# Kernel tuning notes

Hardware: AMD Instinct MI355X
Metric: run time of the kernel (lower is better)

The kernel has to match this reference:

```python
import jax, jax.numpy as jnp
import numpy as np

EPS = 1e-5  # BatchNorm eps (torch default)

def _wq(w):
    # W8A16 fake-quant: per-output-channel symmetric int8 quantize + dequantize
    s = jnp.max(jnp.abs(w), axis=tuple(range(1, w.ndim)), keepdims=True) / 127.0
    s = jnp.maximum(s, 1e-8)
    q = jnp.clip(jnp.round(w / s), -128.0, 127.0)
    return q * s

def _conv(x, w, b, pad):
    y = jax.lax.conv_general_dilated(x, _wq(w), (1, 1), [(pad, pad), (pad, pad)],
                                     dimension_numbers=('NCHW', 'OIHW', 'NCHW'))
    return y + b[None, :, None, None]

def _bn(x, g, b, m, v):
    sh = (1, -1, 1, 1) if x.ndim == 4 else (1, -1)
    inv = jax.lax.rsqrt(v + EPS)
    return (x - m.reshape(sh)) * (inv * g).reshape(sh) + b.reshape(sh)

def _pool(x):
    return jax.lax.reduce_window(x, -jnp.inf, jax.lax.max, (1, 1, 2, 2), (1, 1, 2, 2), 'VALID')

def _ht(x):
    return jnp.clip(x, -1.0, 1.0)

def _linear(x, w, b):
    return x @ _wq(w).T + b

def setup_inputs() -> dict:
    key = jax.random.key(0)
    ks = iter(jax.random.split(key, 64))
    def rn(shape, s=0.05):
        return jax.random.normal(next(ks), shape, jnp.float32) * s
    d = {}
    d['x'] = jax.random.normal(next(ks), (1024, 1, 28, 28), jnp.float32)
    convs = [(1, 32, 5), (32, 64, 5), (64, 128, 3), (128, 256, 3), (256, 256, 1)]
    for i, (ci, co, k) in enumerate(convs, 1):
        d[f'w{i}'] = rn((co, ci, k, k), 0.1)
        d[f'b{i}'] = rn((co,))
        d[f'g{i}'] = jnp.ones((co,), jnp.float32)
        d[f'be{i}'] = jnp.zeros((co,), jnp.float32)
        d[f'mu{i}'] = rn((co,))
        d[f'va{i}'] = jax.random.uniform(next(ks), (co,), jnp.float32, 0.5, 1.5)
    fcs = [(2304, 1024), (1024, 512)]
    for i, (fi, fo) in enumerate(fcs, 1):
        d[f'fw{i}'] = rn((fo, fi), 0.05)
        d[f'fb{i}'] = rn((fo,))
        d[f'fg{i}'] = jnp.ones((fo,), jnp.float32)
        d[f'fbe{i}'] = jnp.zeros((fo,), jnp.float32)
        d[f'fmu{i}'] = rn((fo,))
        d[f'fva{i}'] = jax.random.uniform(next(ks), (fo,), jnp.float32, 0.5, 1.5)
    d['fw3'] = rn((10, 512), 0.05)
    d['fb3'] = rn((10,))
    return d

def reference(x, w1, b1, g1, be1, mu1, va1, w2, b2, g2, be2, mu2, va2,
              w3, b3, g3, be3, mu3, va3, w4, b4, g4, be4, mu4, va4,
              w5, b5, g5, be5, mu5, va5,
              fw1, fb1, fg1, fbe1, fmu1, fva1,
              fw2, fb2, fg2, fbe2, fmu2, fva2, fw3, fb3):
    h = _ht(_bn(_conv(x, w1, b1, 2), g1, be1, mu1, va1))                 # [B,32,28,28]
    h = _ht(_bn(_pool(_conv(h, w2, b2, 2)), g2, be2, mu2, va2))          # [B,64,14,14]
    h = _ht(_bn(_pool(_conv(h, w3, b3, 1)), g3, be3, mu3, va3))          # [B,128,7,7]
    h = _ht(_bn(_pool(_conv(h, w4, b4, 1)), g4, be4, mu4, va4))          # [B,256,3,3]
    h = _ht(_bn(_conv(h, w5, b5, 0), g5, be5, mu5, va5))                 # [B,256,3,3]
    h = h.reshape(h.shape[0], -1)                                        # [B,2304]
    h = _ht(_bn(_linear(h, fw1, fb1), fg1, fbe1, fmu1, fva1))            # [B,1024]
    h = _ht(_bn(_linear(h, fw2, fb2), fg2, fbe2, fmu2, fva2))            # [B,512]
    return _linear(h, fw3, fb3)                                          # [B,10]
```

## Files before the change

kernel.cpp:

```cpp
#include <hip/hip_runtime.h>
#include <hip/hip_bf16.h>
#include <math.h>


#define EPS 1e-5f

typedef __attribute__((ext_vector_type(8))) short bf16x8;
typedef __attribute__((ext_vector_type(4))) float f32x4;
typedef __attribute__((ext_vector_type(16))) float f32x16;
typedef __attribute__((ext_vector_type(4))) int i32x4;

__device__ __forceinline__ short f2bf(float f) {
  unsigned u = __builtin_bit_cast(unsigned, f);
  unsigned r = u + 0x7FFFu + ((u >> 16) & 1u);
  return (short)(r >> 16);
}
__device__ __forceinline__ float bf2f(short h) {
  unsigned u = ((unsigned)(unsigned short)h) << 16;
  return __builtin_bit_cast(float, u);
}
__device__ __forceinline__ int swz2(int pin) {
  return (pin ^ (pin >> 2) ^ (pin >> 5)) & 3;
}
__device__ __forceinline__ int swz3(int pin) {
  return (pin ^ (pin >> 2) ^ (pin >> 4)) & 7;
}
__device__ __forceinline__ float qclip(float w, float s) {
  return fminf(fmaxf(rintf(w / s), -128.f), 127.f);
}

struct PrepArgs {
  const float* w[8];
  short* dsth[8];
  float* dstf;
  float* sc;
  int sco[8];
  int cik[8];
  int kind[8];
  int KK[8];
  int CI[8];
  int OCCH[8];
  int KC[8];
  int cum[9];
};

__global__ __launch_bounds__(256) void prep_all(PrepArgs a) {
  int b = blockIdx.x;
  int t = 0;
  while (b >= a.cum[t + 1]) t++;
  int oc = b - a.cum[t];
  int cik = a.cik[t];
  const float* src = a.w[t] + (size_t)oc * cik;
  float m = 0.f;
  for (int i = threadIdx.x; i < cik; i += 256) m = fmaxf(m, fabsf(src[i]));
  #pragma unroll
  for (int o = 1; o < 64; o <<= 1) m = fmaxf(m, __shfl_xor(m, o));
  __shared__ float red[4];
  __shared__ float ssh;
  if ((threadIdx.x & 63) == 0) red[threadIdx.x >> 6] = m;
  __syncthreads();
  if (threadIdx.x == 0) {
    m = fmaxf(fmaxf(red[0], red[1]), fmaxf(red[2], red[3]));
    float s = fmaxf(m / 127.0f, 1e-8f);
    ssh = s;
    a.sc[a.sco[t] + oc] = s;
  }
  __syncthreads();
  const float s = ssh;
  const int kind = a.kind[t];
  short* dst = a.dsth[t];
  if (kind == 0) {
    for (int tt = threadIdx.x; tt < 32; tt += 256) {
      float q = (tt < 25) ? qclip(src[tt], s) : 0.f;
      dst[(((oc >> 4) * 4 + (tt >> 3)) * 16 + (oc & 15)) * 8 + (tt & 7)] = f2bf(q);
    }
  } else if (kind == 1) {
    const int KK = a.KK[t], CI = a.CI[t], OCCH = a.OCCH[t];
    const int NT32 = OCCH >> 5, KS16 = CI >> 4;
    const int chunk = oc / OCCH, ocl = oc - chunk * OCCH;
    const int nt = ocl >> 5, n32 = ocl & 31;
    for (int idx = threadIdx.x; idx < cik; idx += 256) {
      int ci = idx / KK, kk = idx - ci * KK;
      float q = qclip(src[idx], s);
      int ks = ci >> 4, hh = (ci >> 3) & 1, j = ci & 7;
      size_t d = ((((size_t)(chunk * KK + kk) * NT32 + nt) * KS16 + ks) * 64 +
                  hh * 32 + n32) * 8 + j;
      dst[d] = f2bf(q);
    }
  } else if (kind == 2) {
    const int KK = a.KK[t], CI = a.CI[t], OCCH = a.OCCH[t];
    const int NTC = OCCH >> 4, KS = CI >> 5;
    const int chunk = oc / OCCH, ocl = oc - chunk * OCCH;
    const int ntl = ocl >> 4, mr = ocl & 15;
    for (int idx = threadIdx.x; idx < cik; idx += 256) {
      int ci = idx / KK, kk = idx - ci * KK;
      float q = qclip(src[idx], s);
      int ks = ci >> 5, qq = (ci >> 3) & 3, j = ci & 7;
      size_t d = ((((((size_t)(chunk * KK + kk) * NTC + ntl) * KS + ks) * 4 + qq) *
                   16 + mr)) * 8 + j;
      dst[d] = f2bf(q);
    }
  } else if (kind == 3) {
    const int KC = a.KC[t];
    const int nblk = oc >> 6, ntl = (oc >> 4) & 3, mr = oc & 15;
    for (int k = threadIdx.x; k < cik; k += 256) {
      float q = qclip(src[k], s);
      size_t d = ((((((size_t)nblk * KC + (k >> 7)) * 4 + ntl) * 4 + ((k >> 5) & 3)) *
                   4 + ((k >> 3) & 3)) * 16 + mr) * 8 + (k & 7);
      dst[d] = f2bf(q);
    }
  } else {
    for (int k = threadIdx.x; k < cik; k += 256)
      a.dstf[(size_t)oc * cik + k] = qclip(src[k], s) * s;
  }
}

struct BnArgs {
  const float* p[7][5];
  const float* wsc;
  float* ab;
  int C[7];
  int abo[7];
  int sco[7];
  int cum[8];
};

__global__ __launch_bounds__(256) void bn_all(BnArgs a) {
  int i = blockIdx.x * 256 + threadIdx.x;
  if (i >= a.cum[7]) return;
  int t = 0;
  while (i >= a.cum[t + 1]) t++;
  int c = i - a.cum[t];
  float A = a.p[t][1][c] / sqrtf(a.p[t][4][c] + EPS);
  float B = (a.p[t][0][c] - a.p[t][3][c]) * A + a.p[t][2][c];
  a.ab[a.abo[t] + c] = A * a.wsc[a.sco[t] + c];
  a.ab[a.abo[t] + a.C[t] + c] = B;
}

__global__ __launch_bounds__(448, 2) void conv1_mfma(
    const float* __restrict__ x, const short* __restrict__ wb1,
    const float* __restrict__ ab, short* __restrict__ out) {
  __shared__ __align__(16) float spad[1024];
  __shared__ __align__(16) short sim[784 * 32];
  __shared__ __align__(16) short sw1[1024];
  const int tid = threadIdx.x;
  const int img = blockIdx.x;
  for (int i = tid; i < 1024; i += 448) spad[i] = 0.f;
  for (int i = tid; i < 1024; i += 448) sw1[i] = wb1[i];
  __syncthreads();
  for (int i = tid; i < 784; i += 448)
    spad[(i / 28 + 2) * 32 + (i % 28) + 2] = x[(size_t)img * 784 + i];
  __syncthreads();
  for (int p = tid; p < 784; p += 448) {
    const int py = p / 28, px = p - py * 28;
    const float* sp = &spad[py * 32 + px];
    short v[32];
    #pragma unroll
    for (int ty = 0; ty < 5; ++ty)
      #pragma unroll
      for (int tx = 0; tx < 5; ++tx)
        v[ty * 5 + tx] = f2bf(sp[ty * 32 + tx]);
    #pragma unroll
    for (int j = 25; j < 32; ++j) v[j] = 0;
    #pragma unroll
    for (int j = 0; j < 4; ++j)
      *(bf16x8*)&sim[p * 32 + j * 8] = *(const bf16x8*)&v[j * 8];
  }
  __syncthreads();
  const int lane = tid & 63, wv = tid >> 6;
  const int mrow = lane & 15, quad = lane >> 4;
  f32x4 acc[7][2];
  #pragma unroll
  for (int i = 0; i < 7; ++i) {
    acc[i][0] = (f32x4){0.f, 0.f, 0.f, 0.f};
    acc[i][1] = (f32x4){0.f, 0.f, 0.f, 0.f};
  }
  #pragma unroll
  for (int i = 0; i < 7; ++i) {
    const int mt = wv * 7 + i;
    const bf16x8 a = *(const bf16x8*)&sim[(mt * 16 + mrow) * 32 + quad * 8];
    #pragma unroll
    for (int nt = 0; nt < 2; ++nt) {
      const bf16x8 b = *(const bf16x8*)&sw1[(nt * 4 + quad) * 128 + mrow * 8];
      acc[i][nt] = __builtin_amdgcn_mfma_f32_16x16x32_bf16(a, b, acc[i][nt], 0, 0, 0);
    }
  }
  #pragma unroll
  for (int i = 0; i < 7; ++i) {
    const int mt = wv * 7 + i;
    #pragma unroll
    for (int nt = 0; nt < 2; ++nt) {
      const int oc = nt * 16 + mrow;
      const float A = ab[oc], Bc = ab[32 + oc];
      #pragma unroll
      for (int r = 0; r < 4; ++r) {
        const int p = mt * 16 + quad * 4 + r;
        float v = fminf(fmaxf(acc[i][nt][r] * A + Bc, -1.f), 1.f);
        out[((size_t)img * 784 + p) * 32 + oc] = f2bf(v);
      }
    }
  }
}

__global__ __launch_bounds__(256, 2) void conv2_half(
    const short* __restrict__ in, const short* __restrict__ wfrag,
    const float* __restrict__ ab, short* __restrict__ out) {
  constexpr int S = 4;
  constexpr int RS = 32;
  __shared__ __align__(16) short simg[18 * 32 * 32];
  __shared__ __align__(16) short sw[2][10240];
  const int tid = threadIdx.x;
  const int img = blockIdx.x >> 1, half = blockIdx.x & 1;
  const int lane = tid & 63, wv = tid >> 6;
  const int l31 = lane & 31, h = lane >> 5;

  {
    const int padrow0 = half ? 16 : 0;
    const int vrow0 = half ? 0 : 2;
    for (int c = tid; c < 512; c += 256) {
      int hp = c >> 2, blk = c & 3;
      int pin;
      if (hp < 64) {
        pin = (padrow0 + (hp >> 5)) * RS + (hp & 31);
      } else {
        int r = (hp - 64) >> 2, cc = (hp - 64) & 3;
        int col = (cc < 2) ? cc : (28 + cc);
        pin = (vrow0 + r) * RS + col;
      }
      ((i32x4*)simg)[pin * S + blk] = (i32x4){0, 0, 0, 0};
    }
  }
  {
    const i32x4* gin = (const i32x4*)(in + ((size_t)img * 784 + half * 12 * 28) * 32);
    const int vrow0 = half ? 0 : 2;
    for (int c = tid; c < 1792; c += 256) {
      int ps = c >> 2, blk = c & 3;
      int pin = (vrow0 + ps / 28) * RS + ps % 28 + 2;
      ((i32x4*)simg)[pin * S + (blk ^ swz2(pin))] = gin[c];
    }
  }

  int pinb[4], ppb[4];
  bool uv2[4];
  #pragma unroll
  for (int i = 0; i < 4; ++i) {
    int u = wv + i * 4;
    uv2[i] = u < 13;
    int m = u * 32 + l31;
    int ppl = m >> 2, cd = m & 3;
    bool ok = uv2[i] && (ppl < 98);
    int pr = ppl / 14, pc = ppl - pr * 14;
    int ygl = (half * 7 + pr) * 2 + (cd >> 1);
    int yll = ygl - (half * 14 - 2);
    int xc = pc * 2 + (cd & 1) + 2;
    pinb[i] = ok ? (yll * RS + xc) : (2 * RS + 2);
    ppb[i] = u * 8;
  }

  f32x16 acc[4][2];
  #pragma unroll
  for (int i = 0; i < 4; ++i)
    #pragma unroll
    for (int nt = 0; nt < 2; ++nt)
      #pragma unroll
      for (int e = 0; e < 16; ++e) acc[i][nt][e] = 0.f;

  i32x4 wreg[5];
  {
    const i32x4* ws0 = (const i32x4*)wfrag;
    #pragma unroll
    for (int u2 = 0; u2 < 5; ++u2) wreg[u2] = ws0[tid + u2 * 256];
    #pragma unroll
    for (int u2 = 0; u2 < 5; ++u2) ((i32x4*)sw[0])[tid + u2 * 256] = wreg[u2];
  }

  for (int tg = 0; tg < 5; ++tg) {
    __syncthreads();
    if (tg < 4) {
      const i32x4* ws = (const i32x4*)(wfrag + (size_t)(tg + 1) * 10240);
      #pragma unroll
      for (int u2 = 0; u2 < 5; ++u2) wreg[u2] = ws[tid + u2 * 256];
    }
    const short* swb = sw[tg & 1];
    const int dy = tg - 2;
    #pragma unroll
    for (int tt = 0; tt < 5; ++tt) {
      const int tp = dy * RS + (tt - 2);
      int pin[4], sx4[4];
      #pragma unroll
      for (int i = 0; i < 4; ++i) {
        pin[i] = pinb[i] + tp;
        sx4[i] = swz2(pin[i]);
      }
      #pragma unroll
      for (int ks = 0; ks < 2; ++ks) {
        bf16x8 af[4];
        #pragma unroll
        for (int i = 0; i < 4; ++i)
          af[i] = *(const bf16x8*)&simg[pin[i] * 32 + (((ks * 2 + h) ^ sx4[i]) * 8)];
        #pragma unroll
        for (int nt = 0; nt < 2; ++nt) {
          const bf16x8 bf = *(const bf16x8*)&swb[(((tt * 2 + nt) * 2 + ks) * 64 + lane) * 8];
          #pragma unroll
          for (int i = 0; i < 4; ++i)
            acc[i][nt] = __builtin_amdgcn_mfma_f32_32x32x16_bf16(af[i], bf, acc[i][nt], 0, 0, 0);
        }
      }
    }
    if (tg < 4) {
      #pragma unroll
      for (int u2 = 0; u2 < 5; ++u2)
        ((i32x4*)sw[(tg + 1) & 1])[tid + u2 * 256] = wreg[u2];
    }
  }

  #pragma unroll
  for (int i = 0; i < 4; ++i) {
    #pragma unroll
    for (int nt = 0; nt < 2; ++nt) {
      const int oc = nt * 32 + l31;
      const float A = ab[oc], Bc = ab[64 + oc];
      #pragma unroll
      for (int g = 0; g < 4; ++g) {
        const int ppo = ppb[i] + 2 * g + h;
        if (uv2[i] && ppo < 98) {
          float mx = fmaxf(fmaxf(acc[i][nt][g * 4 + 0], acc[i][nt][g * 4 + 1]),
                           fmaxf(acc[i][nt][g * 4 + 2], acc[i][nt][g * 4 + 3]));
          float v = fminf(fmaxf(mx * A + Bc, -1.f), 1.f);
          out[((size_t)img * 196 + half * 98 + ppo) * 64 + oc] = f2bf(v);
        }
      }
    }
  }
}

__global__ __launch_bounds__(256, 2) void conv3_pad(
    const short* __restrict__ in, const short* __restrict__ wfrag,
    const float* __restrict__ ab, short* __restrict__ out) {
  constexpr int S = 8, RS = 16;
  __shared__ __align__(16) short simg[2 * 256 * 64];
  __shared__ __align__(16) short sw[2][4096];
  const int tid = threadIdx.x;
  const int img0 = blockIdx.x * 2;
  const int lane = tid & 63, wv = tid >> 6;
  const int l31 = lane & 31, h = lane >> 5;

  for (int c = tid; c < 960; c += 256) {
    int blk = c & 7, hp0 = c >> 3;
    int il = hp0 >= 60 ? 1 : 0, hp = hp0 - il * 60;
    int pin;
    if (hp < 32) pin = (hp >> 4) * 15 * RS + (hp & 15);
    else {
      int r = ((hp - 32) >> 1) + 1, cc = ((hp - 32) & 1) * 15;
      pin = r * RS + cc;
    }
    ((i32x4*)simg)[(il * 256 + pin) * S + blk] = (i32x4){0, 0, 0, 0};
  }
  {
    const i32x4* gin = (const i32x4*)(in + (size_t)img0 * 196 * 64);
    for (int c = tid; c < 3136; c += 256) {
      int il = c / 1568, r = c - il * 1568;
      int ps = r >> 3, blk = r & 7;
      int pin = (ps / 14 + 1) * RS + ps % 14 + 1;
      ((i32x4*)simg)[(il * 256 + pin) * S + (blk ^ swz3(pin))] = gin[c];
    }
  }

  int pinb[4], ppb[4], ilv[4];
  bool uv4[4];
  #pragma unroll
  for (int i = 0; i < 4; ++i) {
    int u = wv + i * 4;
    uv4[i] = u < 14;
    int uu = uv4[i] ? u : 0;
    int il = uu / 7, lt = uu - il * 7;
    int m = lt * 32 + l31, ppl = m >> 2, cd = m & 3;
    bool ok = uv4[i] && (ppl < 49);
    int py = ppl / 7, px = ppl - py * 7;
    int y = py * 2 + (cd >> 1), x = px * 2 + (cd & 1);
    pinb[i] = (ok ? ((y + 1) * RS + x + 1) : (RS + 1)) + il * 256;
    ilv[i] = il;
    ppb[i] = lt * 8;
  }

  f32x16 acc[4][2];
  #pragma unroll
  for (int i = 0; i < 4; ++i)
    #pragma unroll
    for (int nt = 0; nt < 2; ++nt)
      #pragma unroll
      for (int e = 0; e < 16; ++e) acc[i][nt][e] = 0.f;

  i32x4 wreg[2];
  {
    const i32x4* ws0 = (const i32x4*)wfrag;
    wreg[0] = ws0[tid];
    wreg[1] = ws0[tid + 256];
    ((i32x4*)sw[0])[tid] = wreg[0];
    ((i32x4*)sw[0])[tid + 256] = wreg[1];
  }

  for (int s = 0; s < 18; ++s) {
    __syncthreads();
    if (s < 17) {
      const i32x4* ws = (const i32x4*)(wfrag + (size_t)(s + 1) * 4096);
      wreg[0] = ws[tid];
      wreg[1] = ws[tid + 256];
    }
    const short* swb = sw[s & 1];
    const int t = s % 9;
    const int tp = (t / 3 - 1) * RS + (t % 3 - 1);
    int pin[4], sx4[4];
    #pragma unroll
    for (int i = 0; i < 4; ++i) {
      pin[i] = pinb[i] + tp;
      sx4[i] = swz3(pin[i]);
    }
    #pragma unroll
    for (int ks = 0; ks < 4; ++ks) {
      bf16x8 af[4];
      #pragma unroll
      for (int i = 0; i < 4; ++i)
        af[i] = *(const bf16x8*)&simg[pin[i] * 64 + (((ks * 2 + h) ^ sx4[i]) * 8)];
      #pragma unroll
      for (int nt = 0; nt < 2; ++nt) {
        const bf16x8 bf = *(const bf16x8*)&swb[((nt * 4 + ks) * 64 + lane) * 8];
        #pragma unroll
        for (int i = 0; i < 4; ++i)
          acc[i][nt] = __builtin_amdgcn_mfma_f32_32x32x16_bf16(af[i], bf, acc[i][nt], 0, 0, 0);
      }
    }
    if (s < 17) {
      ((i32x4*)sw[(s + 1) & 1])[tid] = wreg[0];
      ((i32x4*)sw[(s + 1) & 1])[tid + 256] = wreg[1];
    }
    if (t == 8) {
      const int ch = s / 9;
      #pragma unroll
      for (int i = 0; i < 4; ++i) {
        #pragma unroll
        for (int nt = 0; nt < 2; ++nt) {
          const int oc = ch * 64 + nt * 32 + l31;
          const float A = ab[oc], Bc = ab[128 + oc];
          #pragma unroll
          for (int g = 0; g < 4; ++g) {
            const int ppo = ppb[i] + 2 * g + h;
            if (uv4[i] && ppo < 49) {
              float mx = fmaxf(fmaxf(acc[i][nt][g * 4 + 0], acc[i][nt][g * 4 + 1]),
                               fmaxf(acc[i][nt][g * 4 + 2], acc[i][nt][g * 4 + 3]));
              float v = fminf(fmaxf(mx * A + Bc, -1.f), 1.f);
              out[((size_t)(img0 + ilv[i]) * 49 + ppo) * 128 + oc] = f2bf(v);
            }
          }
          #pragma unroll
          for (int e = 0; e < 16; ++e) acc[i][nt][e] = 0.f;
        }
      }
    }
  }
}

__global__ __launch_bounds__(512, 2) void conv4_mfma(
    const short* __restrict__ in,
    const short* __restrict__ wfrag,
    const float* __restrict__ ab,
    short* __restrict__ outH, short* __restrict__ outL) {
  constexpr int S = 16, NPIX = 49, PP = 9;
  __shared__ __align__(16) short simg[2 * NPIX * 128];
  __shared__ __align__(16) short swb[2][32768];
  const int tid = threadIdx.x;
  const int img0 = blockIdx.x * 2;
  const int lane = tid & 63, wv = tid >> 6;
  const int mrow = lane & 15, quad = lane >> 4;

  {
    const i32x4* gsrc = (const i32x4*)(in + (size_t)img0 * NPIX * 128);
    for (int c = tid; c < 2 * NPIX * S; c += 512) {
      int il = c / (NPIX * S);
      int r = c - il * (NPIX * S);
      int pix = r >> 4, blk = r & 15;
      ((i32x4*)simg)[il * NPIX * S + pix * S + (blk ^ (pix & 15))] = gsrc[c];
    }
    for (int u = tid; u < 4096; u += 512)
      ((i32x4*)swb[0])[u] = ((const i32x4*)wfrag)[u];
  }

  int yy[6], xx[6], ibs[6], ppo_[6], ilv[6];
  bool rv[6], pv[6];
  #pragma unroll
  for (int i = 0; i < 6; ++i) {
    int il = i / 3, lt = i - il * 3;
    int m = lt * 16 + mrow;
    int pp = m >> 2, cd = m & 3;
    rv[i] = pp < PP;
    int py = pp / 3, px = pp - py * 3;
    yy[i] = py * 2 + (cd >> 1);
    xx[i] = px * 2 + (cd & 1);
    ibs[i] = il * NPIX * S;
    ilv[i] = il;
    ppo_[i] = lt * 4 + quad;
    pv[i] = ppo_[i] < PP;
  }
  const int nt0 = wv, nt1 = wv + 8;
  f32x4 acc[6][2];
  #pragma unroll
  for (int i = 0; i < 6; ++i) {
    acc[i][0] = (f32x4){0.f, 0.f, 0.f, 0.f};
    acc[i][1] = (f32x4){0.f, 0.f, 0.f, 0.f};
  }
  __syncthreads();

  int dy = -1, dx = -1;
  for (int t = 0; t < 9; ++t) {
    const int buf = t & 1;
    if (t < 8) {
      const i32x4* wsrc = (const i32x4*)(wfrag + (size_t)(t + 1) * 32768);
      for (int u = tid; u < 4096; u += 512) ((i32x4*)swb[buf ^ 1])[u] = wsrc[u];
    }
    #pragma unroll
    for (int ks = 0; ks < 4; ++ks) {
      bf16x8 af[6];
      #pragma unroll
      for (int i = 0; i < 6; ++i) {
        int iy = yy[i] + dy, ix = xx[i] + dx;
        bool ok = rv[i] && (unsigned)iy < 7u && (unsigned)ix < 7u;
        int pin = iy * 7 + ix;
        int blk = (ks * 4 + quad) ^ (pin & 15);
        af[i] = ok ? *(const bf16x8*)&simg[(ibs[i] + pin * S + blk) * 8]
                   : (bf16x8){0, 0, 0, 0, 0, 0, 0, 0};
      }
      const bf16x8 b0 = *(const bf16x8*)&swb[buf][((nt0 * 4 + ks) * 4 + quad) * 128 + mrow * 8];
      const bf16x8 b1 = *(const bf16x8*)&swb[buf][((nt1 * 4 + ks) * 4 + quad) * 128 + mrow * 8];
      #pragma unroll
      for (int i = 0; i < 6; ++i) {
        acc[i][0] = __builtin_amdgcn_mfma_f32_16x16x32_bf16(af[i], b0, acc[i][0], 0, 0, 0);
        acc[i][1] = __builtin_amdgcn_mfma_f32_16x16x32_bf16(af[i], b1, acc[i][1], 0, 0, 0);
      }
    }
    dx++;
    if (dx == 2) { dx = -1; dy++; }
    __syncthreads();
  }

  #pragma unroll
  for (int i = 0; i < 6; ++i) {
    if (pv[i]) {
      #pragma unroll
      for (int nj = 0; nj < 2; ++nj) {
        const int oc = (nj ? nt1 : nt0) * 16 + mrow;
        const f32x4 a = acc[i][nj];
        float mx = fmaxf(fmaxf(a[0], a[1]), fmaxf(a[2], a[3]));
        float v = fminf(fmaxf(mx * ab[oc] + ab[256 + oc], -1.f), 1.f);
        const int m5 = (img0 + ilv[i]) * 9 + ppo_[i];
        size_t d = ((((((size_t)(m5 >> 6) * 2 + (oc >> 7)) * 4 + ((m5 >> 4) & 3)) * 4 +
                     ((oc >> 5) & 3)) * 4 + ((oc >> 3) & 3)) * 16 + (m5 & 15)) * 8 + (oc & 7);
        short hi = f2bf(v);
        outH[d] = hi;
        outL[d] = f2bf(v - bf2f(hi));
      }
    }
  }
}

template <int KC, int OUTMODE, int KC2, int NALL>
__global__ __launch_bounds__(256, 4) void fc_mfma(
    const short* __restrict__ Xh, const short* __restrict__ Xl,
    const short* __restrict__ Wf, const float* __restrict__ ab,
    float* __restrict__ outF, short* __restrict__ outH, short* __restrict__ outL) {
  const int tid = threadIdx.x;
  const int bn = blockIdx.x, bm = blockIdx.y;
  const int lane = tid & 63, wv = tid >> 6;
  const int mrow = lane & 15, quad = lane >> 4;
  f32x4 acc[4];
  #pragma unroll
  for (int nt = 0; nt < 4; ++nt) acc[nt] = (f32x4){0.f, 0.f, 0.f, 0.f};

  for (int kc = 0; kc < KC; ++kc) {
    const short* xb = Xh + (((size_t)bm * KC + kc) * 4 + wv) * 2048;
    const short* xlb = Xl + (((size_t)bm * KC + kc) * 4 + wv) * 2048;
    const short* wb = Wf + ((size_t)bn * KC + kc) * 8192;
    #pragma unroll
    for (int ks = 0; ks < 4; ++ks) {
      const int ao = ((ks * 4 + quad) * 16 + mrow) * 8;
      const bf16x8 ah = *(const bf16x8*)&xb[ao];
      const bf16x8 al = *(const bf16x8*)&xlb[ao];
      #pragma unroll
      for (int nt = 0; nt < 4; ++nt) {
        const bf16x8 b = *(const bf16x8*)&wb[(((nt * 4 + ks) * 4 + quad) * 16 + mrow) * 8];
        acc[nt] = __builtin_amdgcn_mfma_f32_16x16x32_bf16(ah, b, acc[nt], 0, 0, 0);
        acc[nt] = __builtin_amdgcn_mfma_f32_16x16x32_bf16(al, b, acc[nt], 0, 0, 0);
      }
    }
  }

  #pragma unroll
  for (int nt = 0; nt < 4; ++nt) {
    const int n = bn * 64 + nt * 16 + mrow;
    const float A = ab[n], Bc = ab[NALL + n];
    #pragma unroll
    for (int r = 0; r < 4; ++r) {
      const int m = bm * 64 + wv * 16 + quad * 4 + r;
      float v = fminf(fmaxf(acc[nt][r] * A + Bc, -1.f), 1.f);
      if (OUTMODE == 0) {
        size_t d = (((((((size_t)(m >> 6) * KC2 + (n >> 7)) * 4 + ((m >> 4) & 3)) * 4 +
                       ((n >> 5) & 3)) * 4 + ((n >> 3) & 3)) * 16 + (m & 15))) * 8 + (n & 7);
        short hi = f2bf(v);
        outH[d] = hi;
        outL[d] = f2bf(v - bf2f(hi));
      } else if (OUTMODE == 1) {
        outF[(size_t)m * NALL + n] = v;
      } else {
        const int imgq = m / 9, p = m - imgq * 9;
        const int k1 = n * 9 + p;
        size_t d = ((((((size_t)(imgq >> 6) * KC2 + (k1 >> 7)) * 4 + ((imgq >> 4) & 3)) * 4 +
                     ((k1 >> 5) & 3)) * 4 + ((k1 >> 3) & 3)) * 16 + (imgq & 15)) * 8 + (k1 & 7);
        short hi = f2bf(v);
        outH[d] = hi;
        outL[d] = f2bf(v - bf2f(hi));
      }
    }
  }
}

__global__ __launch_bounds__(256) void fc3_kernel(
    const float* __restrict__ X, const float* __restrict__ W,
    const float* __restrict__ bias, float* __restrict__ out) {
  __shared__ float ws[512 * 10 + 16];
  for (int li = threadIdx.x; li < 5120; li += 256) {
    int n = li / 512, k = li - n * 512;
    ws[k * 10 + n] = W[li];
  }
  __syncthreads();
  const int il = threadIdx.x >> 4, n = threadIdx.x & 15;
  const int img = blockIdx.x * 16 + il;
  if (n < 10) {
    const float4* xp = (const float4*)(X + (size_t)img * 512);
    float s = 0.f;
    for (int k4 = 0; k4 < 128; ++k4) {
      const float4 xv = xp[k4];
      const int k = k4 * 4;
      s += xv.x * ws[k * 10 + n];
      s += xv.y * ws[(k + 1) * 10 + n];
      s += xv.z * ws[(k + 2) * 10 + n];
      s += xv.w * ws[(k + 3) * 10 + n];
    }
    out[img * 10 + n] = s + bias[n];
  }
}

extern "C" void kernel_launch(void* const* d_in, const int* in_sizes, int n_in,
                              void* d_out, int out_size, void* d_ws, size_t ws_size,
                              hipStream_t stream) {
  (void)in_sizes; (void)n_in; (void)out_size; (void)ws_size;
  const float* x = (const float*)d_in[0];
  float* W = (float*)d_ws;

  float* wsc  = W + 0;
  float* ab   = W + 2304;
  float* fq3  = W + 6912;
  short* wb1  = (short*)(W + 12032);
  short* wb2  = (short*)(W + 12544);
  short* wb3  = (short*)(W + 38144);
  short* wb4  = (short*)(W + 75008);
  short* wb5  = (short*)(W + 222464);
  short* fqb1 = (short*)(W + 255232);
  short* fqb2 = (short*)(W + 1434880);
  short* h1   = (short*)(W + 1697024);
  short* h2   = (short*)(W + 14542080);
  short* h3   = (short*)(W + 20964608);
  short* h4h  = (short*)(W + 24175872);
  short* h4l  = (short*)(W + 25355520);
  short* h5h  = (short*)(W + 26535168);
  short* h5l  = (short*)(W + 27714816);
  short* f1h  = (short*)(W + 28894464);
  short* f1l  = (short*)(W + 29418752);
  float* f2   = W + 29943040;

  PrepArgs pa;
  const int widx[8] = {1, 7, 13, 19, 25, 31, 37, 43};
  short* pdst[8] = {wb1, wb2, wb3, wb4, wb5, fqb1, fqb2, nullptr};
  const int sco8[8] = {0, 32, 96, 224, 480, 736, 1760, 2272};
  const int cik8[8] = {25, 800, 576, 1152, 256, 2304, 1024, 512};
  const int co8[8] = {32, 64, 128, 256, 256, 1024, 512, 10};
  const int kind8[8] = {0, 1, 1, 2, 3, 3, 3, 4};
  const int KK8[8] = {25, 25, 9, 9, 1, 1, 1, 1};
  const int CI8[8] = {1, 32, 64, 128, 256, 2304, 1024, 512};
  const int OCCH8[8] = {32, 64, 64, 256, 256, 1024, 512, 10};
  const int KC8[8] = {1, 1, 1, 1, 2, 18, 8, 1};
  int cum = 0;
  for (int i = 0; i < 8; ++i) {
    pa.w[i] = (const float*)d_in[widx[i]];
    pa.dsth[i] = pdst[i];
    pa.sco[i] = sco8[i];
    pa.cik[i] = cik8[i];
    pa.kind[i] = kind8[i];
    pa.KK[i] = KK8[i];
    pa.CI[i] = CI8[i];
    pa.OCCH[i] = OCCH8[i];
    pa.KC[i] = KC8[i];
    pa.cum[i] = cum;
    cum += co8[i];
  }
  pa.cum[8] = cum;
  pa.dstf = fq3;
  pa.sc = wsc;
  hipLaunchKernelGGL(prep_all, dim3(cum), dim3(256), 0, stream, pa);

  BnArgs ba;
  const int bbase[7] = {2, 8, 14, 20, 26, 32, 38};
  const int bc[7] = {32, 64, 128, 256, 256, 1024, 512};
  const int abo[7] = {0, 64, 192, 448, 960, 1472, 3520};
  int bcum = 0;
  for (int t = 0; t < 7; ++t) {
    for (int j = 0; j < 5; ++j) ba.p[t][j] = (const float*)d_in[bbase[t] + j];
    ba.C[t] = bc[t];
    ba.abo[t] = abo[t];
    ba.sco[t] = sco8[t];
    ba.cum[t] = bcum;
    bcum += bc[t];
  }
  ba.cum[7] = bcum;
  ba.ab = ab;
  ba.wsc = wsc;
  hipLaunchKernelGGL(bn_all, dim3((bcum + 255) / 256), dim3(256), 0, stream, ba);

  hipLaunchKernelGGL(conv1_mfma, dim3(1024), dim3(448), 0, stream,
                     x, wb1, ab + 0, h1);
  hipLaunchKernelGGL(conv2_half, dim3(2048), dim3(256), 0, stream,
                     h1, wb2, ab + 64, h2);
  hipLaunchKernelGGL(conv3_pad, dim3(512), dim3(256), 0, stream,
                     h2, wb3, ab + 192, h3);
  hipLaunchKernelGGL(conv4_mfma, dim3(512), dim3(512), 0, stream,
                     h3, wb4, ab + 448, h4h, h4l);
  hipLaunchKernelGGL((fc_mfma<2, 2, 18, 256>), dim3(4, 144), dim3(256), 0, stream,
                     h4h, h4l, wb5, ab + 960, nullptr, h5h, h5l);

  hipLaunchKernelGGL((fc_mfma<18, 0, 8, 1024>), dim3(16, 16), dim3(256), 0, stream,
                     h5h, h5l, fqb1, ab + 1472, nullptr, f1h, f1l);
  hipLaunchKernelGGL((fc_mfma<8, 1, 0, 512>), dim3(8, 16), dim3(256), 0, stream,
                     f1h, f1l, fqb2, ab + 3520, f2, nullptr, nullptr);
  hipLaunchKernelGGL(fc3_kernel, dim3(64), dim3(256), 0, stream,
                     f2, fq3, (const float*)d_in[44], (float*)d_out);
}
```

Baseline: 414.9 us.

## Split-K the FC1 and FC2 MFMA GEMMs with separate combine kernels

Replaces the fused FC1/FC2 GEMM kernels with a split-K variant that writes fp32 partial sums per K slice (3 slices for FC1, 4 for FC2). Small combine kernels then sum the partials and apply the folded BN and hardtanh, writing the hi/lo bf16 tiled layout or fp32. The point is more blocks in flight for these small-grid GEMMs (256 and 128 blocks before) so the GPU is better occupied. The cost is extra global traffic for the partials and two more kernel launches.

```diff
diff --git a/kernel.cpp b/kernel.cpp
--- a/kernel.cpp
+++ b/kernel.cpp
@@ -620,6 +620,73 @@
       }
     }
   }
+}
+
+template <int KC, int KCP, int NALL>
+__global__ __launch_bounds__(256, 4) void fc_mfma_part(
+    const short* __restrict__ Xh, const short* __restrict__ Xl,
+    const short* __restrict__ Wf, float* __restrict__ outP) {
+  const int tid = threadIdx.x;
+  const int bn = blockIdx.x, bm = blockIdx.y, pz = blockIdx.z;
+  const int lane = tid & 63, wv = tid >> 6;
+  const int mrow = lane & 15, quad = lane >> 4;
+  f32x4 acc[4];
+  #pragma unroll
+  for (int nt = 0; nt < 4; ++nt) acc[nt] = (f32x4){0.f, 0.f, 0.f, 0.f};
+
+  const int kc0 = pz * KCP;
+  for (int kc = kc0; kc < kc0 + KCP; ++kc) {
+    const short* xb = Xh + (((size_t)bm * KC + kc) * 4 + wv) * 2048;
+    const short* xlb = Xl + (((size_t)bm * KC + kc) * 4 + wv) * 2048;
+    const short* wb = Wf + ((size_t)bn * KC + kc) * 8192;
+    #pragma unroll
+    for (int ks = 0; ks < 4; ++ks) {
+      const int ao = ((ks * 4 + quad) * 16 + mrow) * 8;
+      const bf16x8 ah = *(const bf16x8*)&xb[ao];
+      const bf16x8 al = *(const bf16x8*)&xlb[ao];
+      #pragma unroll
+      for (int nt = 0; nt < 4; ++nt) {
+        const bf16x8 b = *(const bf16x8*)&wb[(((nt * 4 + ks) * 4 + quad) * 16 + mrow) * 8];
+        acc[nt] = __builtin_amdgcn_mfma_f32_16x16x32_bf16(ah, b, acc[nt], 0, 0, 0);
+        acc[nt] = __builtin_amdgcn_mfma_f32_16x16x32_bf16(al, b, acc[nt], 0, 0, 0);
+      }
+    }
+  }
+
+  const size_t M = (size_t)gridDim.y * 64;
+  float* op = outP + (size_t)pz * M * NALL;
+  #pragma unroll
+  for (int nt = 0; nt < 4; ++nt) {
+    const int n = bn * 64 + nt * 16 + mrow;
+    #pragma unroll
+    for (int r = 0; r < 4; ++r) {
+      const int m = bm * 64 + wv * 16 + quad * 4 + r;
+      op[(size_t)m * NALL + n] = acc[nt][r];
+    }
+  }
+}
+
+__global__ __launch_bounds__(256) void combine_fc1(
+    const float* __restrict__ part, const float* __restrict__ ab,
+    short* __restrict__ outH, short* __restrict__ outL) {
+  int i = blockIdx.x * 256 + threadIdx.x;
+  int m = i >> 10, n = i & 1023;
+  float v = part[i] + part[1048576 + i] + part[2097152 + i];
+  v = fminf(fmaxf(v * ab[n] + ab[1024 + n], -1.f), 1.f);
+  size_t d = (((((((size_t)(m >> 6) * 8 + (n >> 7)) * 4 + ((m >> 4) & 3)) * 4 +
+                 ((n >> 5) & 3)) * 4 + ((n >> 3) & 3)) * 16 + (m & 15))) * 8 + (n & 7);
+  short hi = f2bf(v);
+  outH[d] = hi;
+  outL[d] = f2bf(v - bf2f(hi));
+}
+
+__global__ __launch_bounds__(256) void combine_fc2(
+    const float* __restrict__ part, const float* __restrict__ ab,
+    float* __restrict__ out) {
+  int i = blockIdx.x * 256 + threadIdx.x;
+  int n = i & 511;
+  float v = part[i] + part[524288 + i] + part[1048576 + i] + part[1572864 + i];
+  out[i] = fminf(fmaxf(v * ab[n] + ab[512 + n], -1.f), 1.f);
 }
 
 __global__ __launch_bounds__(256) void fc3_kernel(
@@ -675,6 +742,8 @@
   short* f1h  = (short*)(W + 28894464);
   short* f1l  = (short*)(W + 29418752);
   float* f2   = W + 29943040;
+  float* fp1  = W + 30467328;
+  float* fp2  = W + 33613056;
 
   PrepArgs pa;
   const int widx[8] = {1, 7, 13, 19, 25, 31, 37, 43};
@@ -735,10 +804,14 @@
   hipLaunchKernelGGL((fc_mfma<2, 2, 18, 256>), dim3(4, 144), dim3(256), 0, stream,
                      h4h, h4l, wb5, ab + 960, nullptr, h5h, h5l);
 
-  hipLaunchKernelGGL((fc_mfma<18, 0, 8, 1024>), dim3(16, 16), dim3(256), 0, stream,
-                     h5h, h5l, fqb1, ab + 1472, nullptr, f1h, f1l);
-  hipLaunchKernelGGL((fc_mfma<8, 1, 0, 512>), dim3(8, 16), dim3(256), 0, stream,
-                     f1h, f1l, fqb2, ab + 3520, f2, nullptr, nullptr);
+  hipLaunchKernelGGL((fc_mfma_part<18, 6, 1024>), dim3(16, 16, 3), dim3(256), 0, stream,
+                     h5h, h5l, fqb1, fp1);
+  hipLaunchKernelGGL(combine_fc1, dim3(4096), dim3(256), 0, stream,
+                     fp1, ab + 1472, f1h, f1l);
+  hipLaunchKernelGGL((fc_mfma_part<8, 2, 512>), dim3(8, 16, 4), dim3(256), 0, stream,
+                     f1h, f1l, fqb2, fp2);
+  hipLaunchKernelGGL(combine_fc2, dim3(2048), dim3(256), 0, stream,
+                     fp2, ab + 3520, f2);
   hipLaunchKernelGGL(fc3_kernel, dim3(64), dim3(256), 0, stream,
                      f2, fq3, (const float*)d_in[44], (float*)d_out);
 }
```

New measurement: 411.3 us. About the same (-0.9%).
